# Kernel optimization log

Hardware: AMD Instinct MI355X
Metric: run time of the kernel (lower is better)

Reference implementation:

```python
import jax, jax.numpy as jnp
import numpy as np

XY = 16   # xy_size
Z = 16    # z_size
S = XY * XY * Z   # num_states = 4096
V = 2048  # num_tokens


def _build_structure():
    # Static 3D-grid neighbor structure (replaces the per-state Python loop).
    h = np.arange(S)
    zc, rem = np.divmod(h, XY * XY)
    yc, xc = np.divmod(rem, XY)
    coords = np.stack([xc, yc, zc], 1)                       # [S,3] (x,y,z)
    offs = np.array([[0, 0, 0], [1, 0, 0], [-1, 0, 0], [0, 1, 0],
                     [0, -1, 0], [0, 0, 1], [0, 0, 2]])       # 7 fixed offsets
    nc = coords[:, None, :] + offs[None]                      # [S,7,3]
    valid = ((nc[..., 0] >= 0) & (nc[..., 0] < XY) &
             (nc[..., 1] >= 0) & (nc[..., 1] < XY) &
             (nc[..., 2] >= 0) & (nc[..., 2] < Z))
    dest = nc[..., 0] + XY * (nc[..., 1] + XY * nc[..., 2])   # flat neighbor idx
    # compact valid neighbors to the front, preserving offset order:
    # j-th valid neighbor consumes logit j (matches logits[h, :len(valid)])
    order = np.argsort(~valid, axis=1, kind='stable')
    tgt = np.take_along_axis(dest, order, axis=1)
    vmask = np.take_along_axis(valid, order, axis=1)
    tgt = np.where(vmask, tgt, S)  # invalid slots -> dummy column S
    return jnp.asarray(tgt), jnp.asarray(vmask)

TGT, VMASK = _build_structure()


def transition_log_p(trans_w):
    # masked log-softmax over the first k valid logits of each row
    logits = jnp.where(VMASK, trans_w, -1e30)
    logp = jax.nn.log_softmax(logits, axis=1)
    logp = jnp.where(VMASK, logp, -jnp.inf)
    T = jnp.full((S, S + 1), -jnp.inf, trans_w.dtype)
    T = T.at[jnp.arange(S)[:, None], TGT].set(logp)
    return T[:, :S]  # [S,S], row h = log p(transition targets of h)


def smoothed_emission(emis_w):
    em = jax.nn.log_softmax(emis_w, axis=-1).reshape(Z, XY, XY, V)
    lv, rv = em[:, :, :1], em[:, :, -1:]
    lh, rh = em[:, :1], em[:, -1:]
    c = jnp.zeros((Z, 1, 1, V), em.dtype)  # log(1)=0 pad, as in the original
    c2 = lambda *a: jnp.concatenate(a, axis=2)
    c1 = lambda *a: jnp.concatenate(a, axis=1)
    up = c1(c2(lv, em, rv), c2(c, rh, c), c2(c, rh, c))
    dn = c1(c2(c, lh, c), c2(c, lh, c), c2(lv, em, rv))
    lf = c1(c2(lh, c, c), c2(em, rv, rv), c2(rh, c, c))
    rt = c1(c2(c, c, lh), c2(lv, lv, em), c2(c, c, rh))
    cr = c1(c2(c, lh, c), c2(lv, em, rv), c2(c, rh, c))
    mean = jax.nn.logsumexp(jnp.stack((up, dn, lf, rt, cr)), axis=0) - jnp.log(5.0)
    return mean[:, 1:-1, 1:-1].reshape(S, V)


def _forward(stories, trans_w, emis_w, prior_w):
    priors = jax.nn.log_softmax(prior_w)                      # [S]
    em = smoothed_emission(emis_w)                            # [S,V]
    padded = jnp.concatenate([em, jnp.zeros((S, 1), em.dtype)], axis=1)  # [S,V+1]
    # per-(story, step) emission log-prob: sum over sentence tokens
    all_emis = padded.T[stories].sum(axis=2)                  # [B,L,S]
    all_emis = jnp.transpose(all_emis, (1, 0, 2))             # [L,B,S]
    T = transition_log_p(trans_w)                             # [S,S]
    amax = jnp.max(T, axis=1, keepdims=True)                  # [S,1], finite (self-loop)
    P = jnp.exp(T - amax)                                     # [S,S]
    score0 = all_emis[0] + priors                             # [B,S]

    def step(score, em_t):
        # new[b,a] = em_t[b,a] + logsumexp_h(T[a,h] + score[b,h])  (stable log-matmul)
        smax = jnp.max(score, axis=1, keepdims=True)          # [B,1]
        new = em_t + jnp.log(jnp.exp(score - smax) @ P.T) + smax + amax.T
        return new, new

    _, rest = jax.lax.scan(step, score0, all_emis[1:])
    return jnp.concatenate([score0[None], rest], axis=0)      # [L,B,S]


def setup_inputs() -> dict:
    key = jax.random.key(0)
    k1, k2, k3, k4 = jax.random.split(key, 4)
    B, L, W = 8, 32, 8
    return {
        "stories_tensor": jax.random.randint(k1, (B, L, W), 0, V + 1, dtype=jnp.int32),
        "story_length": L,
        "trans_w": jax.random.normal(k2, (S, 7), jnp.float32),
        "emis_w": jax.random.normal(k3, (S, V), jnp.float32),
        "prior_w": jax.random.normal(k4, (S,), jnp.float32),
    }


def reference(stories_tensor, story_length, trans_w, emis_w, prior_w):
    assert stories_tensor.shape[1] == story_length
    return _forward(stories_tensor, trans_w, emis_w, prior_w)
```

## Files before the change

kernel.cpp:

```cpp
#include <hip/hip_runtime.h>
#include <math.h>

#define XYD 16
#define ZD 16
#define SS 4096
#define VV 2048
#define BB 8
#define LL 32
#define WW 8
#define VC 32
#define SM_STRIDE 257

#define GUARD_L 16
#define GUARD_R 512
#define EBUF_N (GUARD_L + SS + GUARD_R)

__global__ void k_logZ(const float* __restrict__ emis_w, float* __restrict__ logZ) {
    int wave = threadIdx.x >> 6;
    int lane = threadIdx.x & 63;
    int row  = blockIdx.x * 4 + wave;
    const float* r = emis_w + (size_t)row * VV;
    float vals[32];
    float m = -INFINITY;
#pragma unroll
    for (int k = 0; k < 8; k++) {
        float4 f = ((const float4*)r)[k * 64 + lane];
        vals[k*4+0] = f.x; vals[k*4+1] = f.y; vals[k*4+2] = f.z; vals[k*4+3] = f.w;
    }
#pragma unroll
    for (int k = 0; k < 32; k++) m = fmaxf(m, vals[k]);
#pragma unroll
    for (int o = 32; o; o >>= 1) m = fmaxf(m, __shfl_xor(m, o));
    float sum = 0.f;
#pragma unroll
    for (int k = 0; k < 32; k++) sum += __expf(vals[k] - m);
#pragma unroll
    for (int o = 32; o; o >>= 1) sum += __shfl_xor(sum, o);
    if (lane == 0) logZ[row] = m + __logf(sum);
}

__global__ void k_smooth(const float* __restrict__ emis_w, const float* __restrict__ logZ,
                         float* __restrict__ smT) {
    __shared__ float tileT[VC * SM_STRIDE];
    int z  = blockIdx.x;
    int v0 = blockIdx.y * VC;
    int tid = threadIdx.x;
    int rsub = tid >> 3;
    int c0   = (tid & 7) * 4;

#pragma unroll
    for (int it = 0; it < 8; it++) {
        int r  = it * 32 + rsub;
        int sg = z * 256 + r;
        float lz = logZ[sg];
        float4 w = *(const float4*)(emis_w + (size_t)sg * VV + v0 + c0);
        tileT[(c0+0)*SM_STRIDE + r] = __expf(w.x - lz);
        tileT[(c0+1)*SM_STRIDE + r] = __expf(w.y - lz);
        tileT[(c0+2)*SM_STRIDE + r] = __expf(w.z - lz);
        tileT[(c0+3)*SM_STRIDE + r] = __expf(w.w - lz);
    }
    __syncthreads();

    int x = tid & 15, y = tid >> 4;
    int sxp = (x < 15) ? tid + 1  : tid;
    int sxm = (x > 0)  ? tid - 1  : tid;
    int syp = (y < 15) ? tid + 16 : tid;
    int sym = (y > 0)  ? tid - 16 : tid;
    float* o = smT + (size_t)v0 * SS + z * 256 + tid;
#pragma unroll
    for (int i = 0; i < VC; i++) {
        const float* tb = tileT + i * SM_STRIDE;
        float s = tb[tid] + tb[sxp] + tb[sxm] + tb[syp] + tb[sym];
        o[(size_t)i * SS] = __logf(s * 0.2f);
    }
}

__global__ void k_emis(const int* __restrict__ stories, const float* __restrict__ smT,
                       float* __restrict__ all_emis) {
    int blk = blockIdx.x;
    int t = blk >> 3, b = blk & 7;
    int tid = threadIdx.x;
    int tok[WW];
#pragma unroll
    for (int w = 0; w < WW; w++) tok[w] = stories[(b * LL + t) * WW + w];
#pragma unroll
    for (int i = 0; i < 4; i++) {
        int s = i * 1024 + tid * 4;
        float4 acc = {0.f, 0.f, 0.f, 0.f};
#pragma unroll
        for (int w = 0; w < WW; w++) {
            if (tok[w] < VV) {
                float4 f = *(const float4*)(smT + (size_t)tok[w] * SS + s);
                acc.x += f.x; acc.y += f.y; acc.z += f.z; acc.w += f.w;
            }
        }
        *(float4*)(all_emis + ((size_t)t * BB + b) * SS + s) = acc;
    }
}

__global__ void k_trans(const float* __restrict__ trans_w, float* __restrict__ pw_geo,
                        float* __restrict__ am_tab) {
    int j = blockIdx.x * 256 + threadIdx.x;
    int zz = j >> 8, rem = j & 255, yy = rem >> 4, xx = rem & 15;
    bool val[7];
    val[0] = true;
    val[1] = (xx < 15); val[2] = (xx > 0);
    val[3] = (yy < 15); val[4] = (yy > 0);
    val[5] = (zz < 15); val[6] = (zz < 14);
    float raw[7];
#pragma unroll
    for (int k = 0; k < 7; k++) raw[k] = trans_w[j * 7 + k];
    float w[7];
    int cnt = 0;
    float m = -INFINITY;
#pragma unroll
    for (int d = 0; d < 7; d++) {
        if (val[d]) { w[d] = raw[cnt++]; m = fmaxf(m, w[d]); }
    }
    float se = 0.f;
#pragma unroll
    for (int d = 0; d < 7; d++) if (val[d]) se += expf(w[d] - m);
#pragma unroll
    for (int d = 0; d < 7; d++) pw_geo[j * 7 + d] = val[d] ? expf(w[d] - m) : 0.f;
    am_tab[j] = -logf(se);
}

__global__ void __launch_bounds__(1024) k_forward(
    const float* __restrict__ pw_geo, const float* __restrict__ am_tab,
    const float* __restrict__ prior_w, const float* __restrict__ all_emis,
    float* __restrict__ out) {
    __shared__ __align__(16) float Ebuf[2][EBUF_N];
    __shared__ __align__(16) float red[16];
    int b = blockIdx.x;
    int tid = threadIdx.x;
    int lane = tid & 63, wid = tid >> 6;

    if (tid < GUARD_L) { Ebuf[0][tid] = 0.f; Ebuf[1][tid] = 0.f; }
    if (tid < GUARD_R) {
        Ebuf[0][GUARD_L + SS + tid] = 0.f;
        Ebuf[1][GUARD_L + SS + tid] = 0.f;
    }

    union { float4 v4[7]; float f[28]; } U;
    {
        const float4* p4 = (const float4*)(pw_geo) + (size_t)tid * 7;
#pragma unroll
        for (int k = 0; k < 7; k++) U.v4[k] = p4[k];
    }
    float4 am4 = ((const float4*)am_tab)[tid];
    float4 pv  = ((const float4*)prior_w)[tid];

    float lm = fmaxf(fmaxf(pv.x, pv.y), fmaxf(pv.z, pv.w));
#pragma unroll
    for (int o = 32; o; o >>= 1) lm = fmaxf(lm, __shfl_xor(lm, o));
    if (lane == 0) red[wid] = lm;
    __syncthreads();
    float gm = red[0];
#pragma unroll
    for (int w = 1; w < 16; w++) gm = fmaxf(gm, red[w]);
    __syncthreads();
    float ls = __expf(pv.x - gm) + __expf(pv.y - gm) + __expf(pv.z - gm) + __expf(pv.w - gm);
#pragma unroll
    for (int o = 32; o; o >>= 1) ls += __shfl_xor(ls, o);
    if (lane == 0) red[wid] = ls;
    __syncthreads();
    float gs = 0.f;
#pragma unroll
    for (int w = 0; w < 16; w++) gs += red[w];
    float logZp = gm + __logf(gs);
    __syncthreads();

    float4 em0 = ((const float4*)(all_emis + (size_t)b * SS))[tid];
    float v0 = em0.x + pv.x - logZp;
    float v1 = em0.y + pv.y - logZp;
    float v2 = em0.z + pv.z - logZp;
    float v3 = em0.w + pv.w - logZp;
    {
        float4 ov = {v0, v1, v2, v3};
        ((float4*)(out + (size_t)b * SS))[tid] = ov;
    }
    float m = fmaxf(fmaxf(v0, v1), fmaxf(v2, v3));
#pragma unroll
    for (int o = 32; o; o >>= 1) m = fmaxf(m, __shfl_xor(m, o));
    if (lane == 0) red[wid] = m;
    __syncthreads();
    float smax;
    {
        float4 r0 = ((const float4*)red)[0], r1 = ((const float4*)red)[1];
        float4 r2 = ((const float4*)red)[2], r3 = ((const float4*)red)[3];
        smax = fmaxf(fmaxf(fmaxf(r0.x, r0.y), fmaxf(r0.z, r0.w)),
               fmaxf(fmaxf(fmaxf(r1.x, r1.y), fmaxf(r1.z, r1.w)),
               fmaxf(fmaxf(fmaxf(r2.x, r2.y), fmaxf(r2.z, r2.w)),
                     fmaxf(fmaxf(r3.x, r3.y), fmaxf(r3.z, r3.w)))));
    }
    {
        float4 E = {__expf(v0 - smax), __expf(v1 - smax), __expf(v2 - smax), __expf(v3 - smax)};
        ((float4*)(Ebuf[0] + GUARD_L))[tid] = E;
    }
    __syncthreads();

    int cur = 0;
    for (int t = 1; t < LL; t++) {
        const float4* Ep = (const float4*)(Ebuf[cur] + GUARD_L);
        float4 A  = Ep[tid];
        float4 Bx = Ep[tid + 1];
        float4 Cx = Ep[tid - 1];
        float4 Yp = Ep[tid + 4];
        float4 Ym = Ep[tid - 4];
        float4 Zp = Ep[tid + 64];
        float4 Zq = Ep[tid + 128];
        float4 em = ((const float4*)(all_emis + ((size_t)t * BB + b) * SS))[tid];

        float a0 = A.x*U.f[0]  + A.y*U.f[1]  + Cx.w*U.f[2]  + Yp.x*U.f[3]  + Ym.x*U.f[4]  + Zp.x*U.f[5]  + Zq.x*U.f[6];
        float a1 = A.y*U.f[7]  + A.z*U.f[8]  + A.x*U.f[9]   + Yp.y*U.f[10] + Ym.y*U.f[11] + Zp.y*U.f[12] + Zq.y*U.f[13];
        float a2 = A.z*U.f[14] + A.w*U.f[15] + A.y*U.f[16]  + Yp.z*U.f[17] + Ym.z*U.f[18] + Zp.z*U.f[19] + Zq.z*U.f[20];
        float a3 = A.w*U.f[21] + Bx.x*U.f[22]+ A.z*U.f[23]  + Yp.w*U.f[24] + Ym.w*U.f[25] + Zp.w*U.f[26] + Zq.w*U.f[27];

        v0 = em.x + __logf(a0) + smax + am4.x;
        v1 = em.y + __logf(a1) + smax + am4.y;
        v2 = em.z + __logf(a2) + smax + am4.z;
        v3 = em.w + __logf(a3) + smax + am4.w;

        {
            float4 ov = {v0, v1, v2, v3};
            ((float4*)(out + ((size_t)t * BB + b) * SS))[tid] = ov;
        }

        float mm = fmaxf(fmaxf(v0, v1), fmaxf(v2, v3));
#pragma unroll
        for (int o = 32; o; o >>= 1) mm = fmaxf(mm, __shfl_xor(mm, o));
        if (lane == 0) red[wid] = mm;
        __syncthreads();
        {
            float4 r0 = ((const float4*)red)[0], r1 = ((const float4*)red)[1];
            float4 r2 = ((const float4*)red)[2], r3 = ((const float4*)red)[3];
            smax = fmaxf(fmaxf(fmaxf(r0.x, r0.y), fmaxf(r0.z, r0.w)),
                   fmaxf(fmaxf(fmaxf(r1.x, r1.y), fmaxf(r1.z, r1.w)),
                   fmaxf(fmaxf(fmaxf(r2.x, r2.y), fmaxf(r2.z, r2.w)),
                         fmaxf(fmaxf(r3.x, r3.y), fmaxf(r3.z, r3.w)))));
        }
        {
            float4 E = {__expf(v0 - smax), __expf(v1 - smax), __expf(v2 - smax), __expf(v3 - smax)};
            ((float4*)(Ebuf[cur ^ 1] + GUARD_L))[tid] = E;
        }
        __syncthreads();
        cur ^= 1;
    }
}

extern "C" void kernel_launch(void* const* d_in, const int* in_sizes, int n_in,
                              void* d_out, int out_size, void* d_ws, size_t ws_size,
                              hipStream_t stream) {
    const int*   stories = (const int*)d_in[0];
    const float* trans_w = (const float*)d_in[2];
    const float* emis_w  = (const float*)d_in[3];
    const float* prior_w = (const float*)d_in[4];
    float* out = (float*)d_out;

    char* ws = (char*)d_ws;
    float* smT      = (float*)(ws);
    float* all_emis = (float*)(ws + (size_t)VV * SS * 4);
    float* logZ     = (float*)(ws + (size_t)VV * SS * 4 + (size_t)LL * BB * SS * 4);
    float* pw_geo   = (float*)((char*)logZ + SS * 4);
    float* am_tab   = (float*)((char*)pw_geo + (size_t)SS * 7 * 4);

    k_logZ<<<SS / 4, 256, 0, stream>>>(emis_w, logZ);
    k_trans<<<SS / 256, 256, 0, stream>>>(trans_w, pw_geo, am_tab);
    k_smooth<<<dim3(ZD, VV / VC), 256, 0, stream>>>(emis_w, logZ, smT);
    k_emis<<<LL * BB, 256, 0, stream>>>(stories, smT, all_emis);
    k_forward<<<BB, 1024, 0, stream>>>(pw_geo, am_tab, prior_w, all_emis, out);
}
```

Before: 165.8 us.

## Use per-wave local max scaling to drop a barrier per forward step

The forward recursion now normalizes each wave's exp-scores by its own wave-local max and publishes those maxima in shared memory. Consumers rescale neighbor values using the maxima of adjacent waves, which removes the second block-wide barrier per time step. The transition softmax is folded into the forward kernel, eliminating the k_trans launch. The next step's emission row is also prefetched one step ahead. This adds per-neighbor rescaling multiplies and exps, and relies on the neighbor stencil staying within adjacent waves.

```diff
diff --git a/kernel.cpp b/kernel.cpp
--- a/kernel.cpp
+++ b/kernel.cpp
@@ -98,39 +98,12 @@
     }
 }
 
-__global__ void k_trans(const float* __restrict__ trans_w, float* __restrict__ pw_geo,
-                        float* __restrict__ am_tab) {
-    int j = blockIdx.x * 256 + threadIdx.x;
-    int zz = j >> 8, rem = j & 255, yy = rem >> 4, xx = rem & 15;
-    bool val[7];
-    val[0] = true;
-    val[1] = (xx < 15); val[2] = (xx > 0);
-    val[3] = (yy < 15); val[4] = (yy > 0);
-    val[5] = (zz < 15); val[6] = (zz < 14);
-    float raw[7];
-#pragma unroll
-    for (int k = 0; k < 7; k++) raw[k] = trans_w[j * 7 + k];
-    float w[7];
-    int cnt = 0;
-    float m = -INFINITY;
-#pragma unroll
-    for (int d = 0; d < 7; d++) {
-        if (val[d]) { w[d] = raw[cnt++]; m = fmaxf(m, w[d]); }
-    }
-    float se = 0.f;
-#pragma unroll
-    for (int d = 0; d < 7; d++) if (val[d]) se += expf(w[d] - m);
-#pragma unroll
-    for (int d = 0; d < 7; d++) pw_geo[j * 7 + d] = val[d] ? expf(w[d] - m) : 0.f;
-    am_tab[j] = -logf(se);
-}
-
 __global__ void __launch_bounds__(1024) k_forward(
-    const float* __restrict__ pw_geo, const float* __restrict__ am_tab,
-    const float* __restrict__ prior_w, const float* __restrict__ all_emis,
-    float* __restrict__ out) {
+    const float* __restrict__ trans_w, const float* __restrict__ prior_w,
+    const float* __restrict__ all_emis, float* __restrict__ out) {
     __shared__ __align__(16) float Ebuf[2][EBUF_N];
-    __shared__ __align__(16) float red[16];
+    __shared__ float red2[2][20];
+    __shared__ float pr[16];
     int b = blockIdx.x;
     int tid = threadIdx.x;
     int lane = tid & 63, wid = tid >> 6;
@@ -140,110 +113,133 @@
         Ebuf[0][GUARD_L + SS + tid] = 0.f;
         Ebuf[1][GUARD_L + SS + tid] = 0.f;
     }
-
-    union { float4 v4[7]; float f[28]; } U;
+    if (tid < 2) {
+        red2[tid][0]  = -INFINITY; red2[tid][17] = -INFINITY;
+        red2[tid][18] = -INFINITY; red2[tid][19] = -INFINITY;
+    }
+
+    float pw[28], am[4];
     {
-        const float4* p4 = (const float4*)(pw_geo) + (size_t)tid * 7;
-#pragma unroll
-        for (int k = 0; k < 7; k++) U.v4[k] = p4[k];
-    }
-    float4 am4 = ((const float4*)am_tab)[tid];
-    float4 pv  = ((const float4*)prior_w)[tid];
+        float w7[28];
+        const float4* t4 = (const float4*)(trans_w + (size_t)tid * 28);
+#pragma unroll
+        for (int k = 0; k < 7; k++) ((float4*)w7)[k] = t4[k];
+#pragma unroll
+        for (int i = 0; i < 4; i++) {
+            int j = tid * 4 + i;
+            int xx = j & 15, yy = (j >> 4) & 15, zz = j >> 8;
+            bool val[7];
+            val[0] = true;
+            val[1] = (xx < 15); val[2] = (xx > 0);
+            val[3] = (yy < 15); val[4] = (yy > 0);
+            val[5] = (zz < 15); val[6] = (zz < 14);
+            const float* rw = w7 + i * 7;
+            float w[7]; int cnt = 0; float m = -INFINITY;
+#pragma unroll
+            for (int d = 0; d < 7; d++) { if (val[d]) { w[d] = rw[cnt++]; m = fmaxf(m, w[d]); } }
+            float se = 0.f;
+#pragma unroll
+            for (int d = 0; d < 7; d++) if (val[d]) se += __expf(w[d] - m);
+#pragma unroll
+            for (int d = 0; d < 7; d++) pw[i*7+d] = val[d] ? __expf(w[d] - m) : 0.f;
+            am[i] = -__logf(se);
+        }
+    }
+
+    float4 pv = ((const float4*)prior_w)[tid];
+    float4 em = ((const float4*)(all_emis + (size_t)b * SS))[tid];
 
     float lm = fmaxf(fmaxf(pv.x, pv.y), fmaxf(pv.z, pv.w));
 #pragma unroll
     for (int o = 32; o; o >>= 1) lm = fmaxf(lm, __shfl_xor(lm, o));
-    if (lane == 0) red[wid] = lm;
-    __syncthreads();
-    float gm = red[0];
-#pragma unroll
-    for (int w = 1; w < 16; w++) gm = fmaxf(gm, red[w]);
+    if (lane == 0) pr[wid] = lm;
+    __syncthreads();
+    float gm = pr[0];
+#pragma unroll
+    for (int w = 1; w < 16; w++) gm = fmaxf(gm, pr[w]);
     __syncthreads();
     float ls = __expf(pv.x - gm) + __expf(pv.y - gm) + __expf(pv.z - gm) + __expf(pv.w - gm);
 #pragma unroll
     for (int o = 32; o; o >>= 1) ls += __shfl_xor(ls, o);
-    if (lane == 0) red[wid] = ls;
+    if (lane == 0) pr[wid] = ls;
     __syncthreads();
     float gs = 0.f;
 #pragma unroll
-    for (int w = 0; w < 16; w++) gs += red[w];
+    for (int w = 0; w < 16; w++) gs += pr[w];
     float logZp = gm + __logf(gs);
-    __syncthreads();
-
-    float4 em0 = ((const float4*)(all_emis + (size_t)b * SS))[tid];
-    float v0 = em0.x + pv.x - logZp;
-    float v1 = em0.y + pv.y - logZp;
-    float v2 = em0.z + pv.z - logZp;
-    float v3 = em0.w + pv.w - logZp;
-    {
-        float4 ov = {v0, v1, v2, v3};
-        ((float4*)(out + (size_t)b * SS))[tid] = ov;
-    }
-    float m = fmaxf(fmaxf(v0, v1), fmaxf(v2, v3));
-#pragma unroll
-    for (int o = 32; o; o >>= 1) m = fmaxf(m, __shfl_xor(m, o));
-    if (lane == 0) red[wid] = m;
-    __syncthreads();
-    float smax;
-    {
-        float4 r0 = ((const float4*)red)[0], r1 = ((const float4*)red)[1];
-        float4 r2 = ((const float4*)red)[2], r3 = ((const float4*)red)[3];
-        smax = fmaxf(fmaxf(fmaxf(r0.x, r0.y), fmaxf(r0.z, r0.w)),
-               fmaxf(fmaxf(fmaxf(r1.x, r1.y), fmaxf(r1.z, r1.w)),
-               fmaxf(fmaxf(fmaxf(r2.x, r2.y), fmaxf(r2.z, r2.w)),
-                     fmaxf(fmaxf(r3.x, r3.y), fmaxf(r3.z, r3.w)))));
-    }
-    {
-        float4 E = {__expf(v0 - smax), __expf(v1 - smax), __expf(v2 - smax), __expf(v3 - smax)};
-        ((float4*)(Ebuf[0] + GUARD_L))[tid] = E;
-    }
-    __syncthreads();
+
+    float v0 = em.x + pv.x - logZp;
+    float v1 = em.y + pv.y - logZp;
+    float v2 = em.z + pv.z - logZp;
+    float v3 = em.w + pv.w - logZp;
+    { float4 ov = {v0, v1, v2, v3}; ((float4*)(out + (size_t)b * SS))[tid] = ov; }
+    float c = fmaxf(fmaxf(v0, v1), fmaxf(v2, v3));
+#pragma unroll
+    for (int o = 32; o; o >>= 1) c = fmaxf(c, __shfl_xor(c, o));
+    float4 Ereg;
+    Ereg.x = __expf(v0 - c); Ereg.y = __expf(v1 - c);
+    Ereg.z = __expf(v2 - c); Ereg.w = __expf(v3 - c);
+    ((float4*)(Ebuf[0] + GUARD_L))[tid] = Ereg;
+    if (lane == 0) red2[0][1 + wid] = c;
+
+    float4 em_next = ((const float4*)(all_emis + (size_t)BB * SS + (size_t)b * SS))[tid];
 
     int cur = 0;
     for (int t = 1; t < LL; t++) {
-        const float4* Ep = (const float4*)(Ebuf[cur] + GUARD_L);
-        float4 A  = Ep[tid];
-        float4 Bx = Ep[tid + 1];
-        float4 Cx = Ep[tid - 1];
+        __syncthreads();
+        em = em_next;
+        if (t < LL - 1)
+            em_next = ((const float4*)(all_emis + ((size_t)(t + 1) * BB + b) * SS))[tid];
+
+        const float* rr = red2[cur];
+        float c_m1 = rr[wid], c0f = rr[wid + 1], c1f = rr[wid + 2], c2f = rr[wid + 3];
+        bool lo = (lane < 4);
+        float X = fmaxf(fmaxf(c0f, c1f), c2f);
+        if (lo) X = fmaxf(X, c_m1);
+        float f0 = __expf(c0f - X), f1 = __expf(c1f - X), f2 = __expf(c2f - X);
+        float fm1 = lo ? __expf(c_m1 - X) : 0.f;
+
+        const float*  Es = Ebuf[cur] + GUARD_L;
+        const float4* Ep = (const float4*)Es;
+        float  bx  = Es[4 * tid + 4];
+        float  cxw = Es[4 * tid - 1];
         float4 Yp = Ep[tid + 4];
         float4 Ym = Ep[tid - 4];
         float4 Zp = Ep[tid + 64];
         float4 Zq = Ep[tid + 128];
-        float4 em = ((const float4*)(all_emis + ((size_t)t * BB + b) * SS))[tid];
-
-        float a0 = A.x*U.f[0]  + A.y*U.f[1]  + Cx.w*U.f[2]  + Yp.x*U.f[3]  + Ym.x*U.f[4]  + Zp.x*U.f[5]  + Zq.x*U.f[6];
-        float a1 = A.y*U.f[7]  + A.z*U.f[8]  + A.x*U.f[9]   + Yp.y*U.f[10] + Ym.y*U.f[11] + Zp.y*U.f[12] + Zq.y*U.f[13];
-        float a2 = A.z*U.f[14] + A.w*U.f[15] + A.y*U.f[16]  + Yp.z*U.f[17] + Ym.z*U.f[18] + Zp.z*U.f[19] + Zq.z*U.f[20];
-        float a3 = A.w*U.f[21] + Bx.x*U.f[22]+ A.z*U.f[23]  + Yp.w*U.f[24] + Ym.w*U.f[25] + Zp.w*U.f[26] + Zq.w*U.f[27];
-
-        v0 = em.x + __logf(a0) + smax + am4.x;
-        v1 = em.y + __logf(a1) + smax + am4.y;
-        v2 = em.z + __logf(a2) + smax + am4.z;
-        v3 = em.w + __logf(a3) + smax + am4.w;
-
-        {
-            float4 ov = {v0, v1, v2, v3};
-            ((float4*)(out + ((size_t)t * BB + b) * SS))[tid] = ov;
-        }
-
-        float mm = fmaxf(fmaxf(v0, v1), fmaxf(v2, v3));
-#pragma unroll
-        for (int o = 32; o; o >>= 1) mm = fmaxf(mm, __shfl_xor(mm, o));
-        if (lane == 0) red[wid] = mm;
-        __syncthreads();
-        {
-            float4 r0 = ((const float4*)red)[0], r1 = ((const float4*)red)[1];
-            float4 r2 = ((const float4*)red)[2], r3 = ((const float4*)red)[3];
-            smax = fmaxf(fmaxf(fmaxf(r0.x, r0.y), fmaxf(r0.z, r0.w)),
-                   fmaxf(fmaxf(fmaxf(r1.x, r1.y), fmaxf(r1.z, r1.w)),
-                   fmaxf(fmaxf(fmaxf(r2.x, r2.y), fmaxf(r2.z, r2.w)),
-                         fmaxf(fmaxf(r3.x, r3.y), fmaxf(r3.z, r3.w)))));
-        }
-        {
-            float4 E = {__expf(v0 - smax), __expf(v1 - smax), __expf(v2 - smax), __expf(v3 - smax)};
-            ((float4*)(Ebuf[cur ^ 1] + GUARD_L))[tid] = E;
-        }
-        __syncthreads();
+
+        float4 Af;
+        Af.x = Ereg.x * f0; Af.y = Ereg.y * f0; Af.z = Ereg.z * f0; Af.w = Ereg.w * f0;
+        bx  *= (lane == 63) ? f1 : f0;
+        cxw *= (lane == 0)  ? fm1 : f0;
+        float fyp = (lane >= 60) ? f1 : f0;
+        float fym = lo ? fm1 : f0;
+        Yp.x *= fyp; Yp.y *= fyp; Yp.z *= fyp; Yp.w *= fyp;
+        Ym.x *= fym; Ym.y *= fym; Ym.z *= fym; Ym.w *= fym;
+        Zp.x *= f1;  Zp.y *= f1;  Zp.z *= f1;  Zp.w *= f1;
+        Zq.x *= f2;  Zq.y *= f2;  Zq.z *= f2;  Zq.w *= f2;
+
+        float a0 = Af.x*pw[0]  + Af.y*pw[1]  + cxw*pw[2]   + Yp.x*pw[3]  + Ym.x*pw[4]  + Zp.x*pw[5]  + Zq.x*pw[6];
+        float a1 = Af.y*pw[7]  + Af.z*pw[8]  + Af.x*pw[9]  + Yp.y*pw[10] + Ym.y*pw[11] + Zp.y*pw[12] + Zq.y*pw[13];
+        float a2 = Af.z*pw[14] + Af.w*pw[15] + Af.y*pw[16] + Yp.z*pw[17] + Ym.z*pw[18] + Zp.z*pw[19] + Zq.z*pw[20];
+        float a3 = Af.w*pw[21] + bx*pw[22]   + Af.z*pw[23] + Yp.w*pw[24] + Ym.w*pw[25] + Zp.w*pw[26] + Zq.w*pw[27];
+
+        v0 = em.x + __logf(a0) + X + am[0];
+        v1 = em.y + __logf(a1) + X + am[1];
+        v2 = em.z + __logf(a2) + X + am[2];
+        v3 = em.w + __logf(a3) + X + am[3];
+
+        { float4 ov = {v0, v1, v2, v3};
+          ((float4*)(out + ((size_t)t * BB + b) * SS))[tid] = ov; }
+
+        c = fmaxf(fmaxf(v0, v1), fmaxf(v2, v3));
+#pragma unroll
+        for (int o = 32; o; o >>= 1) c = fmaxf(c, __shfl_xor(c, o));
+        Ereg.x = __expf(v0 - c); Ereg.y = __expf(v1 - c);
+        Ereg.z = __expf(v2 - c); Ereg.w = __expf(v3 - c);
+        ((float4*)(Ebuf[cur ^ 1] + GUARD_L))[tid] = Ereg;
+        if (lane == 0) red2[cur ^ 1][1 + wid] = c;
+
         cur ^= 1;
     }
 }
@@ -261,12 +257,9 @@
     float* smT      = (float*)(ws);
     float* all_emis = (float*)(ws + (size_t)VV * SS * 4);
     float* logZ     = (float*)(ws + (size_t)VV * SS * 4 + (size_t)LL * BB * SS * 4);
-    float* pw_geo   = (float*)((char*)logZ + SS * 4);
-    float* am_tab   = (float*)((char*)pw_geo + (size_t)SS * 7 * 4);
 
     k_logZ<<<SS / 4, 256, 0, stream>>>(emis_w, logZ);
-    k_trans<<<SS / 256, 256, 0, stream>>>(trans_w, pw_geo, am_tab);
     k_smooth<<<dim3(ZD, VV / VC), 256, 0, stream>>>(emis_w, logZ, smT);
     k_emis<<<LL * BB, 256, 0, stream>>>(stories, smT, all_emis);
-    k_forward<<<BB, 1024, 0, stream>>>(pw_geo, am_tab, prior_w, all_emis, out);
-}
+    k_forward<<<BB, 1024, 0, stream>>>(trans_w, prior_w, all_emis, out);
+}
```

Result: no change. 167.1 us (+0.8%).
